# Kernel optimization log

Measured on AMD Instinct MI355X. Metric: run time of the kernel, lower is better.

## Reference

```python
import jax, jax.numpy as jnp
import numpy as np


def setup_inputs() -> dict:
    V, D, E = 4096, 128, 12288
    key = jax.random.key(0)
    k1, k2, k3 = jax.random.split(key, 3)
    features = jax.random.normal(k1, (V, D), dtype=jnp.float32)
    # random self-loop-free edge list
    v0 = jax.random.randint(k2, (E,), 0, V)
    off = jax.random.randint(k3, (E,), 1, V)
    v1 = (v0 + off) % V
    edges = jnp.stack([v0, v1]).astype(jnp.int32)  # [2, E]
    # manifold-style neighbor matrix: interior edges share 2 faces
    neighbor = (jnp.zeros((V, V), jnp.int32)
                .at[edges[0], edges[1]].set(2)
                .at[edges[1], edges[0]].set(2))
    return {"features": features, "edges": edges, "neighbor": neighbor}


def _collapse(features, edges, neighbor):
    """Greedy heap-order edge collapse. The heap is built once and only popped,
    so pop order == edges sorted by priority ||f[v0]||^2 + ||f[v1]||^2.
    Returns merge matrix A (f_out = A @ f_in), alive vertex mask, final count."""
    V = neighbor.shape[0]
    target = jnp.int32(V // 2)
    pri = jnp.sum(features * features, axis=1)          # [V]
    epri = pri[edges[0]] + pri[edges[1]]                # [E]
    order = jnp.argsort(epri)                           # heappop order (stable ties)
    alive0 = jnp.ones((V,), bool)
    A0 = jnp.eye(V, dtype=jnp.float32)
    cnt0 = jnp.int32(V)

    def step(carry, e):
        alive, n, A, cnt = carry
        v0 = edges[0, e]
        v1 = edges[1, e]
        do = (cnt > target) & alive[v0] & alive[v1] & (n[v0, v1] == 2)
        # merged neighbor row for v0; v1 dies
        r = (n[v0] + n[v1]).at[v0].set(0).at[v1].set(0)
        row0 = jnp.where(do, r, n[v0])
        row1 = jnp.where(do, jnp.zeros_like(r), n[v1])
        n = (n.at[v0, :].set(row0).at[:, v0].set(row0)
              .at[v1, :].set(row1).at[:, v1].set(row1))
        arow = jnp.where(do, 0.5 * (A[v0] + A[v1]), A[v0])
        A = A.at[v0].set(arow)
        alive = alive.at[v1].set(alive[v1] & jnp.logical_not(do))
        cnt = cnt - do.astype(jnp.int32)
        return (alive, n, A, cnt), None

    (alive, n, A, cnt), _ = jax.lax.scan(step, (alive0, neighbor, A0, cnt0), order)
    return A, alive, cnt


def reference(features, edges, neighbor):
    edges = edges.astype(jnp.int32)
    A, alive, cnt = _collapse(features, edges, neighbor)
    # clean_up() compacts removed vertices; under jit we mask dead rows instead
    pooled = (A @ features) * alive[:, None].astype(features.dtype)
    return pooled, alive, cnt
```

## Files before the change

### kernel.cpp

```cpp
#include <hip/hip_runtime.h>
#include <stdint.h>

#define V 4096
#define D 128
#define E 12288
#define NPAD 16384
#define HALF 8192
#define TARGET 2048
#define MAXM (V - TARGET)
#define ROWU32 256

#define WS_N      0u
#define WS_PRI    (V * ROWU32 * 4u)
#define WS_KEYS   (WS_PRI + V * 4u)
#define WS_PAIRS  (WS_KEYS + NPAD * 8u)
#define WS_MCOUNT (WS_PAIRS + MAXM * 4u)

__global__ void k_scatter(const int* __restrict__ edges, unsigned* __restrict__ n32) {
    int e = blockIdx.x * 256 + threadIdx.x;
    if (e < E) {
        int a = edges[e], b = edges[E + e];
        atomicOr(&n32[a * ROWU32 + (b >> 4)], 2u << ((b & 15) * 2));
        atomicOr(&n32[b * ROWU32 + (a >> 4)], 2u << ((a & 15) * 2));
    }
}

__global__ void k_pri(const float* __restrict__ f, float* __restrict__ pri) {
    int v = blockIdx.x * 256 + threadIdx.x;
    if (v < V) {
        const float* p = f + v * D;
        float r[8];
#pragma unroll
        for (int j = 0; j < 8; j++) r[j] = __fmul_rn(p[j], p[j]);
        for (int i = 8; i < D; i += 8) {
#pragma unroll
            for (int j = 0; j < 8; j++)
                r[j] = __fadd_rn(r[j], __fmul_rn(p[i + j], p[i + j]));
        }
        float s01 = __fadd_rn(r[0], r[1]);
        float s23 = __fadd_rn(r[2], r[3]);
        float s45 = __fadd_rn(r[4], r[5]);
        float s67 = __fadd_rn(r[6], r[7]);
        pri[v] = __fadd_rn(__fadd_rn(s01, s23), __fadd_rn(s45, s67));
    }
}

__launch_bounds__(256)
__global__ void k_main(const int* __restrict__ edges, const float* __restrict__ priG,
                       unsigned* __restrict__ n32, unsigned long long* __restrict__ keys,
                       unsigned* __restrict__ pairsG, int* __restrict__ mcountG,
                       float* __restrict__ out) {
    __shared__ union {
        unsigned long long srt[HALF];
        struct {
            unsigned pk[E];
            uint8_t alive[V];
            unsigned pairs[MAXM];
        } g;
    } sh;
    const int tid = threadIdx.x;

    for (int s = tid; s < NPAD; s += 256) {
        unsigned long long rec;
        if (s < E) {
            int a = edges[s], b = edges[E + s];
            float k = __fadd_rn(priG[a], priG[b]);
            rec = ((unsigned long long)__float_as_uint(k) << 32) | (unsigned)s;
        } else {
            rec = (0xFFFFFFFFull << 32) | (unsigned)s;
        }
        keys[s] = rec;
    }
    __syncthreads();

    for (int h = 0; h < 2; h++) {
        unsigned long long* base = keys + h * HALF;
        for (int s = tid; s < HALF; s += 256) sh.srt[s] = base[s];
        __syncthreads();
        for (int k = 2; k <= HALF; k <<= 1) {
            for (int j = k >> 1; j >= 1; j >>= 1) {
                for (int i = tid; i < HALF; i += 256) {
                    int ixj = i ^ j;
                    if (ixj > i) {
                        unsigned long long a = sh.srt[i], b = sh.srt[ixj];
                        bool up = ((i & k) == 0);
                        if ((a > b) == up) { sh.srt[i] = b; sh.srt[ixj] = a; }
                    }
                }
                __syncthreads();
            }
        }
        for (int s = tid; s < HALF; s += 256) base[s] = sh.srt[s];
        __syncthreads();
    }

    {
        const unsigned long long* A = keys;
        const unsigned long long* B = keys + HALF;
        for (int t = tid; t < (E / 64); t += 256) {
            int d = t * 64;
            int lo = d > HALF ? d - HALF : 0;
            int hi = d < HALF ? d : HALF;
            while (lo < hi) {
                int mid = (lo + hi) >> 1;
                if (A[mid] < B[d - 1 - mid]) lo = mid + 1; else hi = mid;
            }
            int ia = lo, ib = d - lo;
            int end = d + 64; if (end > E) end = E;
            for (int o = d; o < end; o++) {
                bool takeA = (ib >= HALF) || (ia < HALF && A[ia] < B[ib]);
                unsigned long long r = takeA ? A[ia++] : B[ib++];
                int e = (int)(r & 0xFFFFFFFFull);
                int a = edges[e], b = edges[E + e];
                sh.g.pk[o] = ((unsigned)a << 16) | (unsigned)b;
            }
        }
        for (int v = tid; v < V; v += 256) sh.g.alive[v] = 1;
    }
    __syncthreads();

    if (tid < 64) {
        const int lane = tid;
        volatile uint8_t* aliveL = sh.g.alive;
        int cnt = V;
        int mcount = 0;
        bool done = false;
        for (int w = 0; w < E && !done; w += 64) {
            int e = w + lane;
            unsigned pkv = sh.g.pk[e];
            int a = (int)(pkv >> 16), b = (int)(pkv & 0xFFFFu);
            bool av = aliveL[a] && aliveL[b];
            unsigned wv = n32[a * ROWU32 + (b >> 4)];
            unsigned fv = (wv >> ((b & 15) * 2)) & 3u;
            unsigned long long m = __ballot(av && (fv == 2u));
            while (m) {
                int i = __ffsll((unsigned long long)m) - 1;
                int v0 = __shfl(a, i), v1 = __shfl(b, i);

                uint4* rA = (uint4*)(n32 + v0 * ROWU32);
                uint4* rB = (uint4*)(n32 + v1 * ROWU32);
                uint4 ra = rA[lane], rb = rB[lane];
                uint4 rr;
                rr.x = ra.x | rb.x | ((ra.x & rb.x & 0xAAAAAAAAu) >> 1);
                rr.y = ra.y | rb.y | ((ra.y & rb.y & 0xAAAAAAAAu) >> 1);
                rr.z = ra.z | rb.z | ((ra.z & rb.z & 0xAAAAAAAAu) >> 1);
                rr.w = ra.w | rb.w | ((ra.w & rb.w & 0xAAAAAAAAu) >> 1);
                if ((v0 >> 6) == lane) (&rr.x)[(v0 >> 4) & 3] &= ~(3u << ((v0 & 15) * 2));
                if ((v1 >> 6) == lane) (&rr.x)[(v1 >> 4) & 3] &= ~(3u << ((v1 & 15) * 2));
                rA[lane] = rr;
                rB[lane] = make_uint4(0u, 0u, 0u, 0u);

                {
                    int sh0 = (v0 & 15) * 2, sh1 = (v1 & 15) * 2;
                    int wi0 = v0 >> 4, wi1 = v1 >> 4;
#pragma unroll
                    for (int c = 0; c < 4; c++) {
                        unsigned bb = (&rb.x)[c];
                        if (!bb) continue;
                        unsigned aa = (&ra.x)[c];
                        unsigned vv = (&rr.x)[c];
                        int xbase = lane * 64 + c * 16;
                        unsigned t = bb;
                        while (t) {
                            int bit = __ffs(t) - 1;
                            int q = bit >> 1;
                            t &= ~(3u << (q * 2));
                            int x = xbase + q;
                            if (x == v0 || x == v1) continue;
                            unsigned o0  = (aa >> (q * 2)) & 3u;
                            unsigned o1  = (bb >> (q * 2)) & 3u;
                            unsigned val = (vv >> (q * 2)) & 3u;
                            unsigned* base = n32 + x * ROWU32;
                            if (wi0 == wi1) {
                                atomicXor(base + wi0, ((o0 ^ val) << sh0) | (o1 << sh1));
                            } else {
                                unsigned x0 = (o0 ^ val) << sh0;
                                if (x0) atomicXor(base + wi0, x0);
                                atomicXor(base + wi1, o1 << sh1);
                            }
                        }
                    }
                }

                if (lane == 0) {
                    aliveL[v1] = 0;
                    sh.g.pairs[mcount] = ((unsigned)v0 << 16) | (unsigned)v1;
                }
                mcount++;
                cnt--;
                if (cnt == TARGET) { done = true; break; }

                av = av && (a != v1) && (b != v1);
                int tgt = (a == v0) ? b : ((b == v0) ? a : -1);
                int srcl = (tgt >= 0) ? (tgt >> 6) : 0;
                unsigned c0 = __shfl(rr.x, srcl), c1 = __shfl(rr.y, srcl);
                unsigned c2 = __shfl(rr.z, srcl), c3 = __shfl(rr.w, srcl);
                if (tgt >= 0) {
                    int ci = (tgt >> 4) & 3;
                    unsigned cw = (ci == 0) ? c0 : (ci == 1) ? c1 : (ci == 2) ? c2 : c3;
                    fv = (cw >> ((tgt & 15) * 2)) & 3u;
                }
                m = __ballot((lane > i) && av && (fv == 2u));
            }
        }
        for (int p = lane; p < mcount; p += 64) pairsG[p] = sh.g.pairs[p];
        if (lane == 0) mcountG[0] = mcount;
        for (int v = lane; v < V; v += 64)
            out[V * D + v] = sh.g.alive[v] ? 1.0f : 0.0f;
        if (lane == 0) out[V * D + V] = (float)cnt;
    }
}

__launch_bounds__(256)
__global__ void k_apply(const float* __restrict__ f, const unsigned* __restrict__ pairsG,
                        const int* __restrict__ mcountG, float* __restrict__ out) {
    __shared__ unsigned pl[MAXM];
    __shared__ int rootL[256];
    __shared__ float wL[256];
    const int tid = threadIdx.x;
    const int mc = mcountG[0];
    for (int j = tid; j < mc; j += 256) pl[j] = pairsG[j];
    __syncthreads();
    int cur = blockIdx.x * 256 + tid;
    float w = 1.0f;
    for (int j = 0; j < mc; j++) {
        unsigned p = pl[j];
        int v0 = (int)(p >> 16), v1 = (int)(p & 0xFFFFu);
        if (cur == v1) { cur = v0; w *= 0.5f; }
        else if (cur == v0) w *= 0.5f;
    }
    rootL[tid] = cur;
    wL[tid] = w;
    __syncthreads();
    const int sub = tid >> 7;
    const int d = tid & 127;
    for (int s = 0; s < 256; s += 2) {
        int idx = s + sub;
        int vv = blockIdx.x * 256 + idx;
        atomicAdd(&out[rootL[idx] * D + d], wL[idx] * f[vv * D + d]);
    }
}

extern "C" void kernel_launch(void* const* d_in, const int* in_sizes, int n_in,
                              void* d_out, int out_size, void* d_ws, size_t ws_size,
                              hipStream_t stream) {
    (void)in_sizes; (void)n_in; (void)out_size; (void)ws_size;
    const float* features = (const float*)d_in[0];
    const int* edges = (const int*)d_in[1];
    uint8_t* ws = (uint8_t*)d_ws;
    unsigned* n32 = (unsigned*)(ws + WS_N);
    float* pri = (float*)(ws + WS_PRI);
    unsigned long long* keys = (unsigned long long*)(ws + WS_KEYS);
    unsigned* pairsG = (unsigned*)(ws + WS_PAIRS);
    int* mcountG = (int*)(ws + WS_MCOUNT);
    float* out = (float*)d_out;

    hipMemsetAsync(n32, 0, (size_t)V * ROWU32 * 4, stream);
    hipMemsetAsync(out, 0, (size_t)V * D * sizeof(float), stream);
    k_scatter<<<(E + 255) / 256, 256, 0, stream>>>(edges, n32);
    k_pri<<<(V + 255) / 256, 256, 0, stream>>>(features, pri);
    k_main<<<1, 256, 0, stream>>>(edges, pri, n32, keys, pairsG, mcountG, out);
    k_apply<<<V / 256, 256, 0, stream>>>(features, pairsG, mcountG, out);
}
```

Baseline: 4.049 ms.

## Split monolithic kernel and batch independent edge collapses per wavefront step

```diff
diff --git a/kernel.cpp b/kernel.cpp
--- a/kernel.cpp
+++ b/kernel.cpp
@@ -13,8 +13,16 @@
 #define WS_N      0u
 #define WS_PRI    (V * ROWU32 * 4u)
 #define WS_KEYS   (WS_PRI + V * 4u)
-#define WS_PAIRS  (WS_KEYS + NPAD * 8u)
+#define WS_PK     (WS_KEYS + NPAD * 8u)
+#define WS_PAIRS  (WS_PK + E * 4u)
 #define WS_MCOUNT (WS_PAIRS + MAXM * 4u)
+#define WS_ALIVE  (WS_MCOUNT + 16u)
+
+__device__ __forceinline__ unsigned getf(const uint4& r, int c) {
+    unsigned lo = (c & 2) ? r.z : r.x;
+    unsigned hi = (c & 2) ? r.w : r.y;
+    return (c & 1) ? hi : lo;
+}
 
 __global__ void k_scatter(const int* __restrict__ edges, unsigned* __restrict__ n32) {
     int e = blockIdx.x * 256 + threadIdx.x;
@@ -45,170 +53,222 @@
     }
 }
 
-__launch_bounds__(256)
-__global__ void k_main(const int* __restrict__ edges, const float* __restrict__ priG,
-                       unsigned* __restrict__ n32, unsigned long long* __restrict__ keys,
-                       unsigned* __restrict__ pairsG, int* __restrict__ mcountG,
-                       float* __restrict__ out) {
-    __shared__ union {
-        unsigned long long srt[HALF];
-        struct {
-            unsigned pk[E];
-            uint8_t alive[V];
-            unsigned pairs[MAXM];
-        } g;
-    } sh;
-    const int tid = threadIdx.x;
-
-    for (int s = tid; s < NPAD; s += 256) {
+__global__ void k_keys(const int* __restrict__ edges, const float* __restrict__ pri,
+                       unsigned long long* __restrict__ keys) {
+    int s = blockIdx.x * 256 + threadIdx.x;
+    if (s < NPAD) {
         unsigned long long rec;
         if (s < E) {
             int a = edges[s], b = edges[E + s];
-            float k = __fadd_rn(priG[a], priG[b]);
+            float k = __fadd_rn(pri[a], pri[b]);
             rec = ((unsigned long long)__float_as_uint(k) << 32) | (unsigned)s;
         } else {
             rec = (0xFFFFFFFFull << 32) | (unsigned)s;
         }
         keys[s] = rec;
     }
+}
+
+__launch_bounds__(1024)
+__global__ void k_sort2(unsigned long long* __restrict__ keys) {
+    __shared__ unsigned long long srt[HALF];
+    const int tid = threadIdx.x;
+    unsigned long long* base = keys + blockIdx.x * HALF;
+    for (int s = tid; s < HALF; s += 1024) srt[s] = base[s];
     __syncthreads();
-
-    for (int h = 0; h < 2; h++) {
-        unsigned long long* base = keys + h * HALF;
-        for (int s = tid; s < HALF; s += 256) sh.srt[s] = base[s];
-        __syncthreads();
-        for (int k = 2; k <= HALF; k <<= 1) {
-            for (int j = k >> 1; j >= 1; j >>= 1) {
-                for (int i = tid; i < HALF; i += 256) {
-                    int ixj = i ^ j;
-                    if (ixj > i) {
-                        unsigned long long a = sh.srt[i], b = sh.srt[ixj];
-                        bool up = ((i & k) == 0);
-                        if ((a > b) == up) { sh.srt[i] = b; sh.srt[ixj] = a; }
-                    }
-                }
-                __syncthreads();
-            }
+    for (int k = 2; k <= HALF; k <<= 1) {
+        for (int j = k >> 1; j >= 1; j >>= 1) {
+            for (int i = tid; i < HALF; i += 1024) {
+                int ixj = i ^ j;
+                if (ixj > i) {
+                    unsigned long long x = srt[i], y = srt[ixj];
+                    bool up = ((i & k) == 0);
+                    if ((x > y) == up) { srt[i] = y; srt[ixj] = x; }
+                }
+            }
+            __syncthreads();
         }
-        for (int s = tid; s < HALF; s += 256) base[s] = sh.srt[s];
-        __syncthreads();
-    }
-
-    {
-        const unsigned long long* A = keys;
-        const unsigned long long* B = keys + HALF;
-        for (int t = tid; t < (E / 64); t += 256) {
-            int d = t * 64;
-            int lo = d > HALF ? d - HALF : 0;
-            int hi = d < HALF ? d : HALF;
-            while (lo < hi) {
-                int mid = (lo + hi) >> 1;
-                if (A[mid] < B[d - 1 - mid]) lo = mid + 1; else hi = mid;
-            }
-            int ia = lo, ib = d - lo;
-            int end = d + 64; if (end > E) end = E;
-            for (int o = d; o < end; o++) {
-                bool takeA = (ib >= HALF) || (ia < HALF && A[ia] < B[ib]);
-                unsigned long long r = takeA ? A[ia++] : B[ib++];
-                int e = (int)(r & 0xFFFFFFFFull);
-                int a = edges[e], b = edges[E + e];
-                sh.g.pk[o] = ((unsigned)a << 16) | (unsigned)b;
-            }
-        }
-        for (int v = tid; v < V; v += 256) sh.g.alive[v] = 1;
-    }
+    }
+    for (int s = tid; s < HALF; s += 1024) base[s] = srt[s];
+}
+
+__launch_bounds__(64)
+__global__ void k_mergepath(const unsigned long long* __restrict__ keys,
+                            const int* __restrict__ edges, unsigned* __restrict__ pkG) {
+    int t = blockIdx.x * 64 + threadIdx.x;
+    if (t >= E / 64) return;
+    const unsigned long long* A = keys;
+    const unsigned long long* B = keys + HALF;
+    int d = t * 64;
+    int lo = d > HALF ? d - HALF : 0;
+    int hi = d < HALF ? d : HALF;
+    while (lo < hi) {
+        int mid = (lo + hi) >> 1;
+        if (A[mid] < B[d - 1 - mid]) lo = mid + 1; else hi = mid;
+    }
+    int ia = lo, ib = d - lo;
+    for (int o = d; o < d + 64; o++) {
+        bool takeA = (ib >= HALF) || (ia < HALF && A[ia] < B[ib]);
+        unsigned long long r = takeA ? A[ia++] : B[ib++];
+        int e = (int)(r & 0xFFFFFFFFull);
+        int a = edges[e], b = edges[E + e];
+        pkG[o] = ((unsigned)a << 16) | (unsigned)b;
+    }
+}
+
+__launch_bounds__(64)
+__global__ void k_collapse(const unsigned* __restrict__ pkG, unsigned* n32,
+                           unsigned* __restrict__ pairsG, int* __restrict__ mcountG,
+                           uint8_t* __restrict__ aliveG, float* __restrict__ out) {
+    __shared__ uint8_t alive[V];
+    const int lane = threadIdx.x;
+    for (int v = lane; v < V; v += 64) alive[v] = 1;
     __syncthreads();
 
-    if (tid < 64) {
-        const int lane = tid;
-        volatile uint8_t* aliveL = sh.g.alive;
-        int cnt = V;
-        int mcount = 0;
-        bool done = false;
-        for (int w = 0; w < E && !done; w += 64) {
-            int e = w + lane;
-            unsigned pkv = sh.g.pk[e];
-            int a = (int)(pkv >> 16), b = (int)(pkv & 0xFFFFu);
-            bool av = aliveL[a] && aliveL[b];
-            unsigned wv = n32[a * ROWU32 + (b >> 4)];
-            unsigned fv = (wv >> ((b & 15) * 2)) & 3u;
-            unsigned long long m = __ballot(av && (fv == 2u));
-            while (m) {
-                int i = __ffsll((unsigned long long)m) - 1;
-                int v0 = __shfl(a, i), v1 = __shfl(b, i);
-
-                uint4* rA = (uint4*)(n32 + v0 * ROWU32);
-                uint4* rB = (uint4*)(n32 + v1 * ROWU32);
-                uint4 ra = rA[lane], rb = rB[lane];
-                uint4 rr;
-                rr.x = ra.x | rb.x | ((ra.x & rb.x & 0xAAAAAAAAu) >> 1);
-                rr.y = ra.y | rb.y | ((ra.y & rb.y & 0xAAAAAAAAu) >> 1);
-                rr.z = ra.z | rb.z | ((ra.z & rb.z & 0xAAAAAAAAu) >> 1);
-                rr.w = ra.w | rb.w | ((ra.w & rb.w & 0xAAAAAAAAu) >> 1);
-                if ((v0 >> 6) == lane) (&rr.x)[(v0 >> 4) & 3] &= ~(3u << ((v0 & 15) * 2));
-                if ((v1 >> 6) == lane) (&rr.x)[(v1 >> 4) & 3] &= ~(3u << ((v1 & 15) * 2));
-                rA[lane] = rr;
-                rB[lane] = make_uint4(0u, 0u, 0u, 0u);
-
-                {
-                    int sh0 = (v0 & 15) * 2, sh1 = (v1 & 15) * 2;
-                    int wi0 = v0 >> 4, wi1 = v1 >> 4;
+    int cnt = V, mcount = 0;
+    bool done = false;
+
+    for (int w = 0; w < E && !done; w += 64) {
+        unsigned pkv = pkG[w + lane];
+        const int a = (int)(pkv >> 16), b = (int)(pkv & 0xFFFFu);
+        const int widx = a * ROWU32 + (b >> 4);
+        const int wsh = (b & 15) * 2;
+        bool dec = false;
+
+        while (!done) {
+            __builtin_amdgcn_s_waitcnt(0);
+            bool av = alive[a] && alive[b];
+            unsigned wv = ((volatile unsigned*)n32)[widx];
+            bool flag = !dec && av && (((wv >> wsh) & 3u) == 2u);
+            if (!dec && !av) dec = true;
+
+            bool pois = false, vis = false, accMe = false;
+            unsigned long long accMask = 0ull;
+            int nacc = 0;
+            int limit = cnt - TARGET; if (limit > 8) limit = 8;
+            int scanEnd = 64;
+            while (true) {
+                unsigned long long m = __ballot(!dec && !vis && (flag || pois));
+                if (!m) break;
+                int i = __ffsll(m) - 1;
+                unsigned long long pb = __ballot(pois);
+                int ai = __shfl(a, i), bi = __shfl(b, i);
+                bool isP = (pb >> i) & 1ull;
+                if (!isP) {
+                    if (nacc < limit) {
+                        accMask |= 1ull << i; nacc++;
+                        if (lane == i) { dec = true; accMe = true; }
+                    } else { scanEnd = i; break; }
+                } else {
+                    if (lane == i) vis = true;
+                }
+                if (lane > i && (a == ai || a == bi || b == ai || b == bi)) pois = true;
+            }
+            if (!dec && !vis && !pois && !flag && lane < scanEnd) dec = true;
+
+            if (nacc == 0) break;
+
+            uint4 RA[8], RB[8];
+            int MV0[8], MV1[8];
+            {
+                unsigned long long am = accMask;
+#pragma unroll
+                for (int jj = 0; jj < 8; jj++) {
+                    if (jj < nacc) {
+                        int lj = __ffsll(am) - 1; am &= am - 1ull;
+                        int v0 = __shfl(a, lj), v1 = __shfl(b, lj);
+                        MV0[jj] = v0; MV1[jj] = v1;
+                        RA[jj] = *((const uint4*)(n32 + v0 * ROWU32) + lane);
+                        RB[jj] = *((const uint4*)(n32 + v1 * ROWU32) + lane);
+                    }
+                }
+            }
+
+            unsigned keptMask = 0;
+            uint4 RBU = make_uint4(0u, 0u, 0u, 0u);
+#pragma unroll
+            for (int jj = 0; jj < 8; jj++) {
+                if (jj < nacc) {
+                    int v0 = MV0[jj], v1 = MV1[jj];
+                    bool c = false;
+                    if ((v0 >> 6) == lane)
+                        c |= ((getf(RBU, (v0 >> 4) & 3) >> ((v0 & 15) * 2)) & 3u) != 0u;
+                    if ((v1 >> 6) == lane)
+                        c |= ((getf(RBU, (v1 >> 4) & 3) >> ((v1 & 15) * 2)) & 3u) != 0u;
+                    if (__ballot(c) == 0ull) {
+                        keptMask |= 1u << jj;
+                        RBU.x |= RB[jj].x; RBU.y |= RB[jj].y;
+                        RBU.z |= RB[jj].z; RBU.w |= RB[jj].w;
+                    }
+                }
+            }
+            if (accMe) {
+                int myjj = (int)__popcll(accMask & ((1ull << lane) - 1ull));
+                if (!((keptMask >> myjj) & 1u)) dec = false;
+            }
+
+#pragma unroll
+            for (int jj = 0; jj < 8; jj++) {
+                if (jj < nacc && ((keptMask >> jj) & 1u)) {
+                    int v0 = MV0[jj], v1 = MV1[jj];
+                    uint4 ra = RA[jj], rb = RB[jj];
+                    uint4 rr;
+                    rr.x = ra.x | rb.x | ((ra.x & rb.x & 0xAAAAAAAAu) >> 1);
+                    rr.y = ra.y | rb.y | ((ra.y & rb.y & 0xAAAAAAAAu) >> 1);
+                    rr.z = ra.z | rb.z | ((ra.z & rb.z & 0xAAAAAAAAu) >> 1);
+                    rr.w = ra.w | rb.w | ((ra.w & rb.w & 0xAAAAAAAAu) >> 1);
+                    if ((v0 >> 6) == lane) {
+                        unsigned msk = ~(3u << ((v0 & 15) * 2)); int c = (v0 >> 4) & 3;
+                        if (c == 0) rr.x &= msk; else if (c == 1) rr.y &= msk;
+                        else if (c == 2) rr.z &= msk; else rr.w &= msk;
+                    }
+                    if ((v1 >> 6) == lane) {
+                        unsigned msk = ~(3u << ((v1 & 15) * 2)); int c = (v1 >> 4) & 3;
+                        if (c == 0) rr.x &= msk; else if (c == 1) rr.y &= msk;
+                        else if (c == 2) rr.z &= msk; else rr.w &= msk;
+                    }
+                    *((uint4*)(n32 + v0 * ROWU32) + lane) = rr;
+                    int sh0 = (v0 & 15) * 2;
+                    int wi0 = v0 >> 4;
 #pragma unroll
                     for (int c = 0; c < 4; c++) {
-                        unsigned bb = (&rb.x)[c];
+                        unsigned bb = getf(rb, c);
                         if (!bb) continue;
-                        unsigned aa = (&ra.x)[c];
-                        unsigned vv = (&rr.x)[c];
-                        int xbase = lane * 64 + c * 16;
+                        unsigned aa = getf(ra, c);
+                        unsigned vv = getf(rr, c);
+                        int xbase = (lane << 6) + (c << 4);
                         unsigned t = bb;
                         while (t) {
-                            int bit = __ffs(t) - 1;
-                            int q = bit >> 1;
+                            int q = (__ffs(t) - 1) >> 1;
                             t &= ~(3u << (q * 2));
                             int x = xbase + q;
-                            if (x == v0 || x == v1) continue;
-                            unsigned o0  = (aa >> (q * 2)) & 3u;
-                            unsigned o1  = (bb >> (q * 2)) & 3u;
-                            unsigned val = (vv >> (q * 2)) & 3u;
-                            unsigned* base = n32 + x * ROWU32;
-                            if (wi0 == wi1) {
-                                atomicXor(base + wi0, ((o0 ^ val) << sh0) | (o1 << sh1));
-                            } else {
-                                unsigned x0 = (o0 ^ val) << sh0;
-                                if (x0) atomicXor(base + wi0, x0);
-                                atomicXor(base + wi1, o1 << sh1);
+                            if (x != v0 && x != v1) {
+                                unsigned o0  = (aa >> (q * 2)) & 3u;
+                                unsigned val = (vv >> (q * 2)) & 3u;
+                                unsigned dx = (o0 ^ val) << sh0;
+                                if (dx) atomicXor(n32 + x * ROWU32 + wi0, dx);
                             }
                         }
                     }
-                }
-
-                if (lane == 0) {
-                    aliveL[v1] = 0;
-                    sh.g.pairs[mcount] = ((unsigned)v0 << 16) | (unsigned)v1;
-                }
-                mcount++;
-                cnt--;
-                if (cnt == TARGET) { done = true; break; }
-
-                av = av && (a != v1) && (b != v1);
-                int tgt = (a == v0) ? b : ((b == v0) ? a : -1);
-                int srcl = (tgt >= 0) ? (tgt >> 6) : 0;
-                unsigned c0 = __shfl(rr.x, srcl), c1 = __shfl(rr.y, srcl);
-                unsigned c2 = __shfl(rr.z, srcl), c3 = __shfl(rr.w, srcl);
-                if (tgt >= 0) {
-                    int ci = (tgt >> 4) & 3;
-                    unsigned cw = (ci == 0) ? c0 : (ci == 1) ? c1 : (ci == 2) ? c2 : c3;
-                    fv = (cw >> ((tgt & 15) * 2)) & 3u;
-                }
-                m = __ballot((lane > i) && av && (fv == 2u));
-            }
+                    if (lane == 0) {
+                        alive[v1] = 0;
+                        pairsG[mcount] = ((unsigned)v0 << 16) | (unsigned)v1;
+                    }
+                    mcount++; cnt--;
+                }
+            }
+            if (cnt == TARGET) done = true;
+            if (__ballot(!dec) == 0ull) break;
         }
-        for (int p = lane; p < mcount; p += 64) pairsG[p] = sh.g.pairs[p];
-        if (lane == 0) mcountG[0] = mcount;
-        for (int v = lane; v < V; v += 64)
-            out[V * D + v] = sh.g.alive[v] ? 1.0f : 0.0f;
-        if (lane == 0) out[V * D + V] = (float)cnt;
-    }
+    }
+
+    __builtin_amdgcn_s_waitcnt(0);
+    for (int v = lane; v < V; v += 64) {
+        uint8_t ao = alive[v];
+        aliveG[v] = ao;
+        out[V * D + v] = ao ? 1.0f : 0.0f;
+    }
+    if (lane == 0) { mcountG[0] = mcount; out[V * D + V] = (float)cnt; }
 }
 
 __launch_bounds__(256)
@@ -251,14 +311,19 @@
     unsigned* n32 = (unsigned*)(ws + WS_N);
     float* pri = (float*)(ws + WS_PRI);
     unsigned long long* keys = (unsigned long long*)(ws + WS_KEYS);
+    unsigned* pkG = (unsigned*)(ws + WS_PK);
     unsigned* pairsG = (unsigned*)(ws + WS_PAIRS);
     int* mcountG = (int*)(ws + WS_MCOUNT);
+    uint8_t* aliveG = ws + WS_ALIVE;
     float* out = (float*)d_out;
 
     hipMemsetAsync(n32, 0, (size_t)V * ROWU32 * 4, stream);
     hipMemsetAsync(out, 0, (size_t)V * D * sizeof(float), stream);
+    k_pri<<<(V + 255) / 256, 256, 0, stream>>>(features, pri);
     k_scatter<<<(E + 255) / 256, 256, 0, stream>>>(edges, n32);
-    k_pri<<<(V + 255) / 256, 256, 0, stream>>>(features, pri);
-    k_main<<<1, 256, 0, stream>>>(edges, pri, n32, keys, pairsG, mcountG, out);
+    k_keys<<<(NPAD + 255) / 256, 256, 0, stream>>>(edges, pri, keys);
+    k_sort2<<<2, 1024, 0, stream>>>(keys);
+    k_mergepath<<<(E / 64 + 63) / 64, 64, 0, stream>>>(keys, edges, pkG);
+    k_collapse<<<1, 64, 0, stream>>>(pkG, n32, pairsG, mcountG, aliveG, out);
     k_apply<<<V / 256, 256, 0, stream>>>(features, pairsG, mcountG, out);
 }
```

Measured after the change: 3.482 ms. -14.0%, faster.
